# Kernel optimization log

Hardware: AMD Instinct MI355X
Metric: run time of the kernel (lower is better)

## Reference

```python
import jax, jax.numpy as jnp
import numpy as np

D_MODEL = 1024
N_HEADS = 16
FF_DIM = 4096
EPS = 1e-05


def setup_inputs() -> dict:
    key = jax.random.key(0)
    ks = jax.random.split(key, 8)
    B, T, E, F = 4, 2048, D_MODEL, FF_DIM
    s = 0.02
    return {
        "encoder_input": jax.random.normal(ks[0], (B, T, E), jnp.float32),
        "source_padding_masks": jax.random.randint(ks[1], (B, T), 0, 2, jnp.int32),
        "Wq": jax.random.normal(ks[2], (E, E), jnp.float32) * s,
        "Wk": jax.random.normal(ks[3], (E, E), jnp.float32) * s,
        "Wv": jax.random.normal(ks[4], (E, E), jnp.float32) * s,
        "Wo": jax.random.normal(ks[5], (E, E), jnp.float32) * s,
        "w1": jax.random.normal(ks[6], (F, E), jnp.float32) * s,
        "b1": jnp.zeros((F,), jnp.float32),
        "w2": jax.random.normal(ks[7], (E, F), jnp.float32) * s,
        "b2": jnp.zeros((E,), jnp.float32),
        "ln_g": jnp.ones((E,), jnp.float32),
        "ln_b": jnp.zeros((E,), jnp.float32),
    }


def _layer_norm(x, g, b):
    # Faithful to the custom LayerNorm: unbiased std (ddof=1), eps added to sd.
    mean = jnp.mean(x, axis=-1, keepdims=True)
    sd = jnp.std(x, axis=-1, keepdims=True, ddof=1)
    return (x - mean) / (sd + EPS) * g + b


def reference(encoder_input, source_padding_masks, Wq, Wk, Wv, Wo, w1, b1, w2, b2, ln_g, ln_b):
    x = encoder_input
    B, T, E = x.shape
    H, hd = N_HEADS, E // N_HEADS

    q = (x @ Wq.T).reshape(B, T, H, hd).transpose(0, 2, 1, 3)  # [B,H,T,hd]
    k = (x @ Wk.T).reshape(B, T, H, hd).transpose(0, 2, 1, 3)
    v = (x @ Wv.T).reshape(B, T, H, hd).transpose(0, 2, 1, 3)

    scores = jnp.einsum("bhqd,bhkd->bhqk", q, k) / jnp.sqrt(jnp.float32(hd))
    key_mask = source_padding_masks[:, None, None, :]  # [B,1,1,T]
    scores = jnp.where(key_mask == 0, -jnp.inf, scores)
    attn = jax.nn.softmax(scores, axis=-1)
    attn = attn * source_padding_masks[:, None, :, None].astype(attn.dtype)  # query mask post-softmax

    ctx = jnp.einsum("bhqk,bhkd->bhqd", attn, v)
    ctx = ctx.transpose(0, 2, 1, 3).reshape(B, T, E)
    att_out = ctx @ Wo.T

    # residual block 1 (dropout is identity in eval)
    h = _layer_norm(att_out + x, ln_g, ln_b)

    ff = jax.nn.relu(h @ w1.T + b1) @ w2.T + b2
    # residual block 2 (same shared LayerNorm params)
    out = _layer_norm(ff + h, ln_g, ln_b)
    return out
```

## Files before the change

kernel.cpp:

```cpp
#include <hip/hip_runtime.h>
#include <hip/hip_bf16.h>


typedef __attribute__((ext_vector_type(8))) short  short8;
typedef __attribute__((ext_vector_type(4))) float  f32x4;
typedef __attribute__((ext_vector_type(4))) int    i32x4;
typedef __attribute__((ext_vector_type(4))) unsigned short u16x4;

__device__ inline float b2f(unsigned short u) {
    unsigned int x = ((unsigned int)u) << 16;
    return __builtin_bit_cast(float, x);
}
__device__ inline unsigned short f2b(float f) {
    return __builtin_bit_cast(unsigned short, __float2bfloat16(f));
}

__device__ inline void llds16(const unsigned short* g, unsigned short* l) {
    __builtin_amdgcn_global_load_lds(
        (const __attribute__((address_space(1))) unsigned int*)g,
        (__attribute__((address_space(3))) unsigned int*)l, 16, 0, 0);
}

__device__ inline int swz(int row, int col8) {
    return (row << 6) + (((col8 ^ (row >> 1)) & 7) << 3);
}

struct CastArgs {
    const float* src[7];
    unsigned short* dst[7];
    int blkcum[8];
};

__global__ __launch_bounds__(256)
void cast_all(CastArgs a)
{
    int blk = blockIdx.x;
    int s = 0;
    while (blk >= a.blkcum[s + 1]) ++s;
    int i = (blk - a.blkcum[s]) * 256 + threadIdx.x;
    f32x4 v = *(const f32x4*)(a.src[s] + (size_t)i * 4);
    u16x4 o;
    for (int j = 0; j < 4; ++j) o[j] = f2b(v[j]);
    *(u16x4*)(a.dst[s] + (size_t)i * 4) = o;
}

__global__ __launch_bounds__(256)
void mask_bf16(const int* __restrict__ m, unsigned short* __restrict__ mb, int n)
{
    int i = blockIdx.x * 256 + threadIdx.x;
    if (i < n) mb[i] = m[i] ? (unsigned short)0x3F80 : (unsigned short)0;
}

template <int BIAS, int RELU, int QKV>
__global__ __launch_bounds__(256, 2)
void gemm_db(const unsigned short* __restrict__ A,
             const unsigned short* __restrict__ W,
             const float* __restrict__ bias,
             const int* __restrict__ mask,
             unsigned short* __restrict__ C0,
             unsigned short* __restrict__ C1,
             unsigned short* __restrict__ C2,
             int M, int N, int K)
{
    __shared__ __attribute__((aligned(16))) unsigned short a_s[2][128 * 64];
    __shared__ __attribute__((aligned(16))) unsigned short b_s[2][128 * 64];

    const int tid  = threadIdx.x;
    const int lane = tid & 63;
    const int w    = tid >> 6;
    const int ln   = lane & 15;
    const int quad = lane >> 4;
    const int wm   = w >> 1, wn = w & 1;
    const int bm   = blockIdx.y, bn = blockIdx.x;

    f32x4 acc[4][4] = {};

    const unsigned short* Abase = A + (size_t)(bm * 128) * K;
    const unsigned short* Wbase = W + (size_t)(bn * 128) * K;

    auto stage = [&](int buf, int kt) {
#pragma unroll
        for (int i = 0; i < 4; ++i) {
            int e   = i * 256 + tid;
            int row = e >> 3;
            int c8  = (e & 7) ^ ((e >> 4) & 7);
            llds16(Abase + (size_t)row * K + kt * 64 + c8 * 8, &a_s[buf][e * 8]);
            llds16(Wbase + (size_t)row * K + kt * 64 + c8 * 8, &b_s[buf][e * 8]);
        }
    };

    const int nkt = K >> 6;
    stage(0, 0);
    stage(1, 1);
    int cur = 0;
    for (int kt = 0; kt < nkt; ++kt) {
        if (kt + 1 < nkt) asm volatile("s_waitcnt vmcnt(8)" ::: "memory");
        else              asm volatile("s_waitcnt vmcnt(0)" ::: "memory");
        asm volatile("s_barrier" ::: "memory");
#pragma unroll
        for (int ks = 0; ks < 2; ++ks) {
            short8 af[4], bf_[4];
#pragma unroll
            for (int mt = 0; mt < 4; ++mt)
                af[mt] = *(const short8*)&a_s[cur][swz(wm * 64 + mt * 16 + ln, ks * 4 + quad)];
#pragma unroll
            for (int nt = 0; nt < 4; ++nt)
                bf_[nt] = *(const short8*)&b_s[cur][swz(wn * 64 + nt * 16 + ln, ks * 4 + quad)];
#pragma unroll
            for (int mt = 0; mt < 4; ++mt)
#pragma unroll
                for (int nt = 0; nt < 4; ++nt)
                    acc[mt][nt] = __builtin_amdgcn_mfma_f32_16x16x32_bf16(
                        af[mt], bf_[nt], acc[mt][nt], 0, 0, 0);
        }
        asm volatile("s_barrier" ::: "memory");
        if (kt + 2 < nkt) stage(cur, kt + 2);
        cur ^= 1;
    }

    if (QKV) {
        const int seg = bn >> 3;
        const int lbn = bn & 7;
        if (seg < 2) {
            unsigned short* C = seg == 0 ? C0 : C1;
#pragma unroll
            for (int nt = 0; nt < 4; ++nt) {
                int col = lbn * 128 + wn * 64 + nt * 16 + ln;
#pragma unroll
                for (int mt = 0; mt < 4; ++mt) {
                    int row0 = bm * 128 + wm * 64 + mt * 16 + quad * 4;
#pragma unroll
                    for (int r = 0; r < 4; ++r)
                        C[(size_t)(row0 + r) * 1024 + col] = f2b(acc[mt][nt][r]);
                }
            }
        } else {
            const int T2 = 2048, H2 = 16;
#pragma unroll
            for (int mt = 0; mt < 4; ++mt) {
                int row0 = bm * 128 + wm * 64 + mt * 16 + quad * 4;
                int bb = row0 >> 11, t0 = row0 & 2047;
                i32x4 mi = *(const i32x4*)&mask[bb * 2048 + t0];
#pragma unroll
                for (int nt = 0; nt < 4; ++nt) {
                    int col = lbn * 128 + wn * 64 + nt * 16 + ln;
                    int hh2 = col >> 6, d = col & 63;
                    u16x4 o;
#pragma unroll
                    for (int r = 0; r < 4; ++r)
                        o[r] = mi[r] ? f2b(acc[mt][nt][r]) : (unsigned short)0;
                    *(u16x4*)(C2 + ((size_t)((bb * H2 + hh2) * 64 + d)) * T2 + t0) = o;
                }
            }
        }
    } else {
#pragma unroll
        for (int nt = 0; nt < 4; ++nt) {
            int col = bn * 128 + wn * 64 + nt * 16 + ln;
            float bv = 0.f;
            if (BIAS) bv = bias[col];
#pragma unroll
            for (int mt = 0; mt < 4; ++mt) {
                int row0 = bm * 128 + wm * 64 + mt * 16 + quad * 4;
#pragma unroll
                for (int r = 0; r < 4; ++r) {
                    float v = acc[mt][nt][r] + bv;
                    if (RELU) v = v > 0.f ? v : 0.f;
                    C0[(size_t)(row0 + r) * N + col] = f2b(v);
                }
            }
        }
    }
}

__global__ __launch_bounds__(512, 2)
void flash_attn3(const unsigned short* __restrict__ Q,
                 const unsigned short* __restrict__ K,
                 const unsigned short* __restrict__ Vt,
                 const unsigned short* __restrict__ mb,
                 const int* __restrict__ mask,
                 unsigned short* __restrict__ O,
                 int T, int H, int E)
{
    __shared__ __attribute__((aligned(16))) unsigned short k_s[2][64 * 64];
    __shared__ __attribute__((aligned(16))) unsigned short v_s[2][64 * 64];
    __shared__ __attribute__((aligned(16))) unsigned short p_s[128 * 64];

    const int ord = blockIdx.x;
    const int wg  = (ord & 7) * 128 + (ord >> 3);
    const int qt  = wg & 15;
    const int h   = (wg >> 4) & 15;
    const int b   = wg >> 8;

    const int tid  = threadIdx.x;
    const int w    = tid >> 6;
    const int lane = tid & 63;
    const int ln   = lane & 15;
    const int quad = lane >> 4;
    const int q0   = qt * 128;
    const unsigned short* vt_b = Vt + (size_t)(b * H + h) * 64 * T;

    {
        int e = tid;
        int row = e >> 3;
        int c8  = (e & 7) ^ ((e >> 4) & 7);
        llds16(K + (size_t)(b * T + row) * E + h * 64 + c8 * 8, &k_s[0][e * 8]);
        llds16(vt_b + (size_t)row * T + c8 * 8, &v_s[0][e * 8]);
    }
    for (int i = 0; i < 2; ++i) {
        int e = i * 512 + tid;
        int row = e >> 3;
        int c8  = (e & 7) ^ ((e >> 4) & 7);
        llds16(Q + (size_t)(b * T + q0 + row) * E + h * 64 + c8 * 8, &p_s[e * 8]);
    }
    __syncthreads();
    short8 aq[2];
    aq[0] = *(const short8*)&p_s[w * 1024 + swz(ln, quad)];
    aq[1] = *(const short8*)&p_s[w * 1024 + swz(ln, 4 + quad)];

    f32x4 Oa[4] = {};
    f32x4 lacc = {};
    const float SCL = 0.125f * 1.44269504f;

    const int nkb = T >> 6;
    for (int kb = 0; kb < nkb; ++kb) {
        const int cur = kb & 1;
        if (kb + 1 < nkb) {
            int e = tid;
            int row = e >> 3;
            int c8  = (e & 7) ^ ((e >> 4) & 7);
            llds16(K + (size_t)(b * T + (kb + 1) * 64 + row) * E + h * 64 + c8 * 8,
                   &k_s[cur ^ 1][e * 8]);
            llds16(vt_b + (size_t)row * T + (kb + 1) * 64 + c8 * 8,
                   &v_s[cur ^ 1][e * 8]);
        }
        short8 mf0 = *(const short8*)&mb[b * T + kb * 64 + quad * 8];
        short8 mf1 = *(const short8*)&mb[b * T + kb * 64 + 32 + quad * 8];

        f32x4 S[4] = {};
        for (int ks = 0; ks < 2; ++ks)
            for (int nt = 0; nt < 4; ++nt) {
                short8 bf_ = *(const short8*)&k_s[cur][swz(nt * 16 + ln, ks * 4 + quad)];
                S[nt] = __builtin_amdgcn_mfma_f32_16x16x32_bf16(aq[ks], bf_, S[nt], 0, 0, 0);
            }
        for (int nt = 0; nt < 4; ++nt)
            for (int r = 0; r < 4; ++r) {
                float p = exp2f(S[nt][r] * SCL);
                p_s[w * 1024 + swz(quad * 4 + r, 2 * nt + (ln >> 3)) + (ln & 7)] = f2b(p);
            }
        short8 ap0 = *(const short8*)&p_s[w * 1024 + swz(ln, quad)];
        short8 ap1 = *(const short8*)&p_s[w * 1024 + swz(ln, 4 + quad)];
        lacc = __builtin_amdgcn_mfma_f32_16x16x32_bf16(ap0, mf0, lacc, 0, 0, 0);
        lacc = __builtin_amdgcn_mfma_f32_16x16x32_bf16(ap1, mf1, lacc, 0, 0, 0);
        for (int nt = 0; nt < 4; ++nt) {
            short8 bv0 = *(const short8*)&v_s[cur][swz(nt * 16 + ln, quad)];
            Oa[nt] = __builtin_amdgcn_mfma_f32_16x16x32_bf16(ap0, bv0, Oa[nt], 0, 0, 0);
            short8 bv1 = *(const short8*)&v_s[cur][swz(nt * 16 + ln, 4 + quad)];
            Oa[nt] = __builtin_amdgcn_mfma_f32_16x16x32_bf16(ap1, bv1, Oa[nt], 0, 0, 0);
        }
        __syncthreads();
    }

    for (int r = 0; r < 4; ++r) {
        int qrow = q0 + w * 16 + quad * 4 + r;
        float inv = mask[b * T + qrow] ? 1.f / lacc[r] : 0.f;
        for (int nt = 0; nt < 4; ++nt)
            O[(size_t)(b * T + qrow) * E + h * 64 + nt * 16 + ln] = f2b(Oa[nt][r] * inv);
    }
}

template <int R_F32, int O_F32>
__global__ __launch_bounds__(256, 4)
void ln_residual(const unsigned short* __restrict__ A,
                 const void* __restrict__ R,
                 const float* __restrict__ G,
                 const float* __restrict__ Bt,
                 void* __restrict__ Y, int E)
{
    const int row = blockIdx.x;
    const int tid = threadIdx.x;
    size_t base = (size_t)row * E + tid * 4;
    u16x4 a4 = *(const u16x4*)(A + base);
    float rv[4];
    if (R_F32) {
        f32x4 r4 = *(const f32x4*)((const float*)R + base);
        for (int j = 0; j < 4; ++j) rv[j] = r4[j];
    } else {
        u16x4 r4 = *(const u16x4*)((const unsigned short*)R + base);
        for (int j = 0; j < 4; ++j) rv[j] = b2f(r4[j]);
    }
    float v[4]; float s = 0.f, sq = 0.f;
    for (int j = 0; j < 4; ++j) {
        v[j] = b2f(a4[j]) + rv[j];
        s += v[j]; sq += v[j] * v[j];
    }
    for (int o = 32; o; o >>= 1) {
        s  += __shfl_xor(s, o, 64);
        sq += __shfl_xor(sq, o, 64);
    }
    __shared__ float red[8];
    int w = tid >> 6, lane = tid & 63;
    if (lane == 0) { red[w] = s; red[4 + w] = sq; }
    __syncthreads();
    s  = red[0] + red[1] + red[2] + red[3];
    sq = red[4] + red[5] + red[6] + red[7];
    float mean = s / E;
    float var  = (sq - s * mean) / (E - 1);
    var = fmaxf(var, 0.f);
    float inv = 1.f / (sqrtf(var) + 1e-5f);
    f32x4 g4 = *(const f32x4*)(G + tid * 4);
    f32x4 b4 = *(const f32x4*)(Bt + tid * 4);
    if (O_F32) {
        f32x4 o4;
        for (int j = 0; j < 4; ++j)
            o4[j] = (v[j] - mean) * inv * g4[j] + b4[j];
        *(f32x4*)((float*)Y + base) = o4;
    } else {
        u16x4 o4;
        for (int j = 0; j < 4; ++j)
            o4[j] = f2b((v[j] - mean) * inv * g4[j] + b4[j]);
        *(u16x4*)((unsigned short*)Y + base) = o4;
    }
}

extern "C" void kernel_launch(void* const* d_in, const int* in_sizes, int n_in,
                              void* d_out, int out_size, void* d_ws, size_t ws_size,
                              hipStream_t stream)
{
    const int B = 4, T = 2048, E = 1024, F = 4096, H = 16;
    const int M = B * T;

    const float* x  = (const float*)d_in[0];
    const int* mask = (const int*)d_in[1];
    const float* Wq = (const float*)d_in[2];
    const float* Wk = (const float*)d_in[3];
    const float* Wv = (const float*)d_in[4];
    const float* Wo = (const float*)d_in[5];
    const float* w1 = (const float*)d_in[6];
    const float* b1 = (const float*)d_in[7];
    const float* w2 = (const float*)d_in[8];
    const float* b2 = (const float*)d_in[9];
    const float* lg = (const float*)d_in[10];
    const float* lb = (const float*)d_in[11];
    float* out = (float*)d_out;

    char* ws = (char*)d_ws;
    const size_t MB = 1024 * 1024;
    unsigned short* xb  = (unsigned short*)(ws);
    unsigned short* q   = (unsigned short*)(ws + 16 * MB);
    unsigned short* kk  = (unsigned short*)(ws + 32 * MB);
    unsigned short* vt  = (unsigned short*)(ws + 48 * MB);
    unsigned short* ctx = (unsigned short*)(ws + 64 * MB);
    unsigned short* hh  = (unsigned short*)(ws + 80 * MB);
    unsigned short* mbf = hh;
    unsigned short* ff1 = (unsigned short*)(ws);
    unsigned short* ff2 = ctx;
    unsigned short* att = q;
    unsigned short* Wqb = (unsigned short*)(ws + 96 * MB);
    unsigned short* Wkb = (unsigned short*)(ws + 98 * MB);
    unsigned short* Wvb = (unsigned short*)(ws + 100 * MB);
    unsigned short* Wob = (unsigned short*)(ws + 102 * MB);
    unsigned short* w1b = (unsigned short*)(ws + 104 * MB);
    unsigned short* w2b = (unsigned short*)(ws + 112 * MB);

    dim3 blk(256);
    dim3 g512(512);

    CastArgs ca;
    ca.src[0] = x;  ca.dst[0] = xb;
    ca.src[1] = Wq; ca.dst[1] = Wqb;
    ca.src[2] = Wk; ca.dst[2] = Wkb;
    ca.src[3] = Wv; ca.dst[3] = Wvb;
    ca.src[4] = Wo; ca.dst[4] = Wob;
    ca.src[5] = w1; ca.dst[5] = w1b;
    ca.src[6] = w2; ca.dst[6] = w2b;
    int blks[7] = { M * E / 1024, E * E / 1024, E * E / 1024, E * E / 1024,
                    E * E / 1024, F * E / 1024, F * E / 1024 };
    ca.blkcum[0] = 0;
    for (int i = 0; i < 7; ++i) ca.blkcum[i + 1] = ca.blkcum[i] + blks[i];
    cast_all<<<dim3(ca.blkcum[7]), blk, 0, stream>>>(ca);
    mask_bf16<<<dim3(M / 256), blk, 0, stream>>>(mask, mbf, M);

    gemm_db<0, 0, 1><<<dim3(3072 / 128, M / 128), blk, 0, stream>>>(
        xb, Wqb, nullptr, mask, q, kk, vt, M, 3072, E);
    flash_attn3<<<dim3((T / 128) * H * B), g512, 0, stream>>>(q, kk, vt, mbf, mask, ctx, T, H, E);
    gemm_db<0, 0, 0><<<dim3(E / 128, M / 128), blk, 0, stream>>>(
        ctx, Wob, nullptr, nullptr, att, nullptr, nullptr, M, E, E);
    ln_residual<1, 0><<<dim3(M), blk, 0, stream>>>(att, x, lg, lb, hh, E);
    gemm_db<1, 1, 0><<<dim3(F / 128, M / 128), blk, 0, stream>>>(
        hh, w1b, b1, nullptr, ff1, nullptr, nullptr, M, F, E);
    gemm_db<1, 0, 0><<<dim3(E / 128, M / 128), blk, 0, stream>>>(
        ff1, w2b, b2, nullptr, ff2, nullptr, nullptr, M, E, F);
    ln_residual<0, 1><<<dim3(M), blk, 0, stream>>>(ff2, hh, lg, lb, out, E);
}
```

Baseline: 520.8 us.

## Fold softmax scale into Q projection and shrink attention P buffer

Multiplies Q by the softmax scale and log2(e) in the QKV GEMM epilogue, so the attention kernel no longer multiplies every score. Q fragments are loaded straight from global memory into registers instead of being staged through LDS. The per-wave P scratch is cut to half-width (16x32) and reused for two halves of the K block, with exponentiation and PV MFMAs interleaved per half. Together with launch_bounds raised to 8, the smaller LDS footprint is meant to allow more resident blocks, at the cost of extra register pressure and bf16 rounding of the prescaled Q.

```diff
diff --git a/kernel.cpp b/kernel.cpp
--- a/kernel.cpp
+++ b/kernel.cpp
@@ -123,6 +123,7 @@
         const int lbn = bn & 7;
         if (seg < 2) {
             unsigned short* C = seg == 0 ? C0 : C1;
+            const float scl = seg == 0 ? 0.18033688f : 1.0f;
 #pragma unroll
             for (int nt = 0; nt < 4; ++nt) {
                 int col = lbn * 128 + wn * 64 + nt * 16 + ln;
@@ -131,7 +132,7 @@
                     int row0 = bm * 128 + wm * 64 + mt * 16 + quad * 4;
 #pragma unroll
                     for (int r = 0; r < 4; ++r)
-                        C[(size_t)(row0 + r) * 1024 + col] = f2b(acc[mt][nt][r]);
+                        C[(size_t)(row0 + r) * 1024 + col] = f2b(acc[mt][nt][r] * scl);
                 }
             }
         } else {
@@ -173,8 +174,8 @@
     }
 }
 
-__global__ __launch_bounds__(512, 2)
-void flash_attn3(const unsigned short* __restrict__ Q,
+__global__ __launch_bounds__(512, 8)
+void flash_attn6(const unsigned short* __restrict__ Q,
                  const unsigned short* __restrict__ K,
                  const unsigned short* __restrict__ Vt,
                  const unsigned short* __restrict__ mb,
@@ -184,7 +185,7 @@
 {
     __shared__ __attribute__((aligned(16))) unsigned short k_s[2][64 * 64];
     __shared__ __attribute__((aligned(16))) unsigned short v_s[2][64 * 64];
-    __shared__ __attribute__((aligned(16))) unsigned short p_s[128 * 64];
+    __shared__ __attribute__((aligned(16))) unsigned short p_s[8][512];
 
     const int ord = blockIdx.x;
     const int wg  = (ord & 7) * 128 + (ord >> 3);
@@ -200,6 +201,11 @@
     const int q0   = qt * 128;
     const unsigned short* vt_b = Vt + (size_t)(b * H + h) * 64 * T;
 
+    const unsigned short* qp = Q + (size_t)(b * T + q0 + w * 16 + ln) * E + h * 64;
+    short8 aq[2];
+    aq[0] = *(const short8*)(qp + quad * 8);
+    aq[1] = *(const short8*)(qp + 32 + quad * 8);
+
     {
         int e = tid;
         int row = e >> 3;
@@ -207,20 +213,12 @@
         llds16(K + (size_t)(b * T + row) * E + h * 64 + c8 * 8, &k_s[0][e * 8]);
         llds16(vt_b + (size_t)row * T + c8 * 8, &v_s[0][e * 8]);
     }
-    for (int i = 0; i < 2; ++i) {
-        int e = i * 512 + tid;
-        int row = e >> 3;
-        int c8  = (e & 7) ^ ((e >> 4) & 7);
-        llds16(Q + (size_t)(b * T + q0 + row) * E + h * 64 + c8 * 8, &p_s[e * 8]);
-    }
     __syncthreads();
-    short8 aq[2];
-    aq[0] = *(const short8*)&p_s[w * 1024 + swz(ln, quad)];
-    aq[1] = *(const short8*)&p_s[w * 1024 + swz(ln, 4 + quad)];
 
     f32x4 Oa[4] = {};
     f32x4 lacc = {};
-    const float SCL = 0.125f * 1.44269504f;
+    unsigned short* ph = &p_s[w][0];
+    const int rdoff = ln * 32 + (((quad ^ (ln >> 1)) & 3) << 3);
 
     const int nkb = T >> 6;
     for (int kb = 0; kb < nkb; ++kb) {
@@ -243,18 +241,30 @@
                 short8 bf_ = *(const short8*)&k_s[cur][swz(nt * 16 + ln, ks * 4 + quad)];
                 S[nt] = __builtin_amdgcn_mfma_f32_16x16x32_bf16(aq[ks], bf_, S[nt], 0, 0, 0);
             }
-        for (int nt = 0; nt < 4; ++nt)
+
+        for (int nt = 0; nt < 2; ++nt)
             for (int r = 0; r < 4; ++r) {
-                float p = exp2f(S[nt][r] * SCL);
-                p_s[w * 1024 + swz(quad * 4 + r, 2 * nt + (ln >> 3)) + (ln & 7)] = f2b(p);
-            }
-        short8 ap0 = *(const short8*)&p_s[w * 1024 + swz(ln, quad)];
-        short8 ap1 = *(const short8*)&p_s[w * 1024 + swz(ln, 4 + quad)];
+                float p = exp2f(S[nt][r]);
+                int qr = quad * 4 + r;
+                int k8 = 2 * nt + (ln >> 3);
+                ph[qr * 32 + (((k8 ^ (qr >> 1)) & 3) << 3) + (ln & 7)] = f2b(p);
+            }
+        short8 ap0 = *(const short8*)&ph[rdoff];
         lacc = __builtin_amdgcn_mfma_f32_16x16x32_bf16(ap0, mf0, lacc, 0, 0, 0);
-        lacc = __builtin_amdgcn_mfma_f32_16x16x32_bf16(ap1, mf1, lacc, 0, 0, 0);
         for (int nt = 0; nt < 4; ++nt) {
             short8 bv0 = *(const short8*)&v_s[cur][swz(nt * 16 + ln, quad)];
             Oa[nt] = __builtin_amdgcn_mfma_f32_16x16x32_bf16(ap0, bv0, Oa[nt], 0, 0, 0);
+        }
+        for (int nt = 0; nt < 2; ++nt)
+            for (int r = 0; r < 4; ++r) {
+                float p = exp2f(S[2 + nt][r]);
+                int qr = quad * 4 + r;
+                int k8 = 2 * nt + (ln >> 3);
+                ph[qr * 32 + (((k8 ^ (qr >> 1)) & 3) << 3) + (ln & 7)] = f2b(p);
+            }
+        short8 ap1 = *(const short8*)&ph[rdoff];
+        lacc = __builtin_amdgcn_mfma_f32_16x16x32_bf16(ap1, mf1, lacc, 0, 0, 0);
+        for (int nt = 0; nt < 4; ++nt) {
             short8 bv1 = *(const short8*)&v_s[cur][swz(nt * 16 + ln, 4 + quad)];
             Oa[nt] = __builtin_amdgcn_mfma_f32_16x16x32_bf16(ap1, bv1, Oa[nt], 0, 0, 0);
         }
@@ -383,7 +393,7 @@
 
     gemm_db<0, 0, 1><<<dim3(3072 / 128, M / 128), blk, 0, stream>>>(
         xb, Wqb, nullptr, mask, q, kk, vt, M, 3072, E);
-    flash_attn3<<<dim3((T / 128) * H * B), g512, 0, stream>>>(q, kk, vt, mbf, mask, ctx, T, H, E);
+    flash_attn6<<<dim3((T / 128) * H * B), g512, 0, stream>>>(q, kk, vt, mbf, mask, ctx, T, H, E);
     gemm_db<0, 0, 0><<<dim3(E / 128, M / 128), blk, 0, stream>>>(
         ctx, Wob, nullptr, nullptr, att, nullptr, nullptr, M, E, E);
     ln_residual<1, 0><<<dim3(M), blk, 0, stream>>>(att, x, lg, lb, hh, E);
```

Result: no change. 514.0 us (-1.3%).
